# Performance work log

Measured on AMD Instinct MI355X. Metric: run time of the kernel, lower is better.

## Reference

```python
import jax, jax.numpy as jnp
import numpy as np

B, N, C = 8, 3072, 768
NUM_HEADS, NUM_DIL, KS = 12, 3, 3


def setup_inputs() -> dict:
    key = jax.random.key(0)
    k1, k2, k3 = jax.random.split(key, 3)
    x = jax.random.normal(k1, (B, N, C), dtype=jnp.float32)
    qkv_w = jax.random.normal(k2, (3 * C, C), dtype=jnp.float32) * 0.02
    proj_w = jax.random.normal(k3, (C, C), dtype=jnp.float32) * 0.02
    proj_b = jnp.zeros((C,), dtype=jnp.float32)
    return {"x": x, "qkv_w": qkv_w, "proj_w": proj_w, "proj_b": proj_b}


def reference(x, qkv_w, proj_w, proj_b):
    Bx, Nx, Cx = x.shape
    nd, ks, heads = NUM_DIL, KS, NUM_HEADS
    hd = Cx // heads          # head_dim = 64
    d = Cx // nd              # channels per dilation = 256
    h = heads // nd           # heads per dilation = 4
    nb = Nx // ks             # number of windows along N
    scale = hd ** -0.5

    # qkv: [B,N,3C] -> [nd,3,B,d,N] (matches torch permute(3,2,0,4,1))
    qkv = (x @ qkv_w.T).reshape(Bx, Nx, 3, nd, d)
    qkv = jnp.transpose(qkv, (3, 2, 0, 4, 1))
    q, k, v = qkv[:, 0], qkv[:, 1], qkv[:, 2]  # each [nd,B,d,N]

    def split_heads(t):
        # [nd,B,d,N] -> [nd,B,h,hd,ks,nb] -> [nd,B,h,nb,ks,hd]
        t = t.reshape(nd, Bx, h, hd, ks, nb)
        return jnp.transpose(t, (0, 1, 2, 5, 4, 3))

    qh = split_heads(q)
    kh = split_heads(k)
    vh = split_heads(v)

    # tiny per-window attention: [nd,B,h,nb,ks,ks]
    attn = jnp.einsum('nbhwqd,nbhwkd->nbhwqk', qh, kh) * scale
    attn = jax.nn.softmax(attn, axis=-1)
    out = jnp.einsum('nbhwqk,nbhwkd->nbhwqd', attn, vh)  # [nd,B,h,nb,ks,hd]

    # torch: transpose(1,2).reshape(B,N,d) per dilation, then permute(1,2,0,3).reshape(B,N,C)
    out = jnp.transpose(out, (0, 1, 3, 2, 4, 5)).reshape(nd, Bx, Nx, d)
    out = jnp.transpose(out, (1, 2, 0, 3)).reshape(Bx, Nx, Cx)
    return out @ proj_w.T + proj_b
```

## Files before the change

### kernel.cpp

```cpp
#include <hip/hip_runtime.h>
#include <stdint.h>

#define DEVFN __device__ __forceinline__

typedef unsigned short u16;
typedef __bf16 bf16_t;
typedef bf16_t bf16x8 __attribute__((ext_vector_type(8)));
typedef float  f32x4  __attribute__((ext_vector_type(4)));

static constexpr int Bb = 8, Nn = 3072, Cc = 768;
static constexpr int Mr = Bb * Nn;
static constexpr int C3 = 3 * Cc;
static constexpr int NB = 1024;

DEVFN u16 f2bf_rne(float f) {
  uint32_t u = __builtin_bit_cast(uint32_t, f);
  u += 0x7FFFu + ((u >> 16) & 1u);
  return (u16)(u >> 16);
}
DEVFN float bf2f(u16 v) {
  uint32_t u = ((uint32_t)v) << 16;
  return __builtin_bit_cast(float, u);
}

__global__ void cvt_f32_bf16(const float4* __restrict__ in, ushort4* __restrict__ out, int n4) {
  int i = blockIdx.x * blockDim.x + threadIdx.x;
  int stride = gridDim.x * blockDim.x;
  for (; i < n4; i += stride) {
    float4 v = in[i];
    ushort4 o;
    o.x = f2bf_rne(v.x); o.y = f2bf_rne(v.y);
    o.z = f2bf_rne(v.z); o.w = f2bf_rne(v.w);
    out[i] = o;
  }
}

DEVFN void gload_lds16(const void* g, void* l) {
  __builtin_amdgcn_global_load_lds(
      (const __attribute__((address_space(1))) uint32_t*)g,
      (__attribute__((address_space(3))) uint32_t*)l,
      16, 0, 0);
}

template <bool OUT_F32>
__global__ __launch_bounds__(512, 2)
void gemm256(const u16* __restrict__ A, const u16* __restrict__ Bw,
             void* __restrict__ Cout, const float* __restrict__ bias,
             int Ndim, int K) {
  constexpr int SLOT = 32768;
  __shared__ char lds[4 * SLOT];

  const int nTn = Ndim >> 8;
  const int nwg = gridDim.x;
  const int bid = blockIdx.x;
  const int wgid = (bid & 7) * (nwg >> 3) + (bid >> 3);
  const int tm = wgid / nTn, tn = wgid % nTn;

  const int t = threadIdx.x;
  const int l = t & 63;
  const int w = t >> 6;
  const int wr = w >> 2;
  const int wcq = w & 3;
  const int lr = l & 15;

  const int NPH = K >> 5;

  const int srow = l >> 2;
  const int scol = 8 * ((l & 3) ^ (srow & 3));
  const u16* pA0 = A  + (size_t)(tm * 256 +       w * 16 + srow) * K + scol;
  const u16* pA1 = A  + (size_t)(tm * 256 + 128 + w * 16 + srow) * K + scol;
  const u16* pB0 = Bw + (size_t)(tn * 256 +       w * 16 + srow) * K + scol;
  const u16* pB1 = Bw + (size_t)(tn * 256 + 128 + w * 16 + srow) * K + scol;

  const int lane_off = lr * 64 + (((l >> 4) * 16) ^ ((lr & 3) << 4));

  f32x4 acc[8][4];
  #pragma unroll
  for (int m = 0; m < 8; ++m)
    #pragma unroll
    for (int n = 0; n < 4; ++n)
      acc[m][n] = f32x4{0.f, 0.f, 0.f, 0.f};

  #pragma unroll
  for (int q = 0; q < 3; ++q) {
    char* dA = &lds[q * SLOT + w * 1024];
    char* dB = &lds[q * SLOT + 16384 + w * 1024];
    const size_t ko = (size_t)q * 32;
    gload_lds16(pA0 + ko, dA);
    gload_lds16(pA1 + ko, dA + 8192);
    gload_lds16(pB0 + ko, dB);
    gload_lds16(pB1 + ko, dB + 8192);
  }

#define GPHASE(VMSTR, PF_COND)                                                \
  do {                                                                        \
    asm volatile(VMSTR ::: "memory");                                         \
    __builtin_amdgcn_s_barrier();                                             \
    asm volatile("" ::: "memory");                                            \
    const char* ab = &lds[(p & 3) * SLOT] + wr * 8192 + lane_off;             \
    const char* bb = &lds[(p & 3) * SLOT + 16384] + wcq * 4096 + lane_off;    \
    bf16x8 af[8], bf[4];                                                      \
    _Pragma("unroll")                                                         \
    for (int m = 0; m < 8; ++m)                                               \
      af[m] = *reinterpret_cast<const bf16x8*>(ab + m * 1024);                \
    _Pragma("unroll")                                                         \
    for (int n = 0; n < 4; ++n)                                               \
      bf[n] = *reinterpret_cast<const bf16x8*>(bb + n * 1024);                \
    if (PF_COND) {                                                            \
      const int ps = (p + 3) & 3;                                             \
      char* dA = &lds[ps * SLOT + w * 1024];                                  \
      char* dB = &lds[ps * SLOT + 16384 + w * 1024];                          \
      const size_t ko = (size_t)(p + 3) * 32;                                 \
      gload_lds16(pA0 + ko, dA);                                              \
      gload_lds16(pA1 + ko, dA + 8192);                                       \
      gload_lds16(pB0 + ko, dB);                                              \
      gload_lds16(pB1 + ko, dB + 8192);                                       \
    }                                                                         \
    __builtin_amdgcn_s_setprio(1);                                            \
    _Pragma("unroll")                                                         \
    for (int m = 0; m < 8; ++m)                                               \
      _Pragma("unroll")                                                       \
      for (int n = 0; n < 4; ++n)                                             \
        acc[m][n] = __builtin_amdgcn_mfma_f32_16x16x32_bf16(af[m], bf[n],     \
                                                            acc[m][n], 0,0,0);\
    __builtin_amdgcn_s_setprio(0);                                            \
    asm volatile("" ::: "memory");                                            \
  } while (0)

  int p = 0;
  for (; p < NPH - 2; ++p) GPHASE("s_waitcnt vmcnt(8)", (p + 3 < NPH));
  GPHASE("s_waitcnt vmcnt(4)", false); ++p;
  GPHASE("s_waitcnt vmcnt(0)", false); ++p;
#undef GPHASE

  const int rb = tm * 256 + wr * 128 + (l >> 4) * 4;
  const int cbase = tn * 256 + wcq * 64 + lr;
  #pragma unroll
  for (int m = 0; m < 8; ++m) {
    #pragma unroll
    for (int n = 0; n < 4; ++n) {
      const int col = cbase + n * 16;
      const int row0 = rb + m * 16;
      if constexpr (OUT_F32) {
        float* O = (float*)Cout;
        const float bv = bias[col];
        #pragma unroll
        for (int j = 0; j < 4; ++j)
          O[(size_t)(row0 + j) * Ndim + col] = acc[m][n][j] + bv;
      } else {
        u16* O = (u16*)Cout;
        #pragma unroll
        for (int j = 0; j < 4; ++j)
          O[(size_t)(row0 + j) * Ndim + col] = f2bf_rne(acc[m][n][j]);
      }
    }
  }
}

__global__ __launch_bounds__(256)
void attn_local(const u16* __restrict__ qkv, u16* __restrict__ y) {
  const int t = threadIdx.x;
  const int wv = t >> 6, lane = t & 63;
  int wid = blockIdx.x * 4 + wv;
  const int w = wid & (NB - 1); wid >>= 10;
  const int head = wid & 3; wid >>= 2;
  const int b = wid & 7; wid >>= 3;
  const int dil = wid;

  const int colq = dil * 256 + head * 64 + lane;
  float q[3], k[3], v[3];
  #pragma unroll
  for (int i = 0; i < 3; ++i) {
    const size_t row = (size_t)(b * Nn + i * NB + w) * C3;
    q[i] = bf2f(qkv[row + colq]);
    k[i] = bf2f(qkv[row + 768 + colq]);
    v[i] = bf2f(qkv[row + 1536 + colq]);
  }

  float s[3][3];
  #pragma unroll
  for (int i = 0; i < 3; ++i)
    #pragma unroll
    for (int j = 0; j < 3; ++j) {
      float p = q[i] * k[j];
      #pragma unroll
      for (int off = 32; off > 0; off >>= 1)
        p += __shfl_xor(p, off, 64);
      s[i][j] = p * 0.125f;
    }

  #pragma unroll
  for (int i = 0; i < 3; ++i) {
    const float mx = fmaxf(fmaxf(s[i][0], s[i][1]), s[i][2]);
    const float e0 = __expf(s[i][0] - mx);
    const float e1 = __expf(s[i][1] - mx);
    const float e2 = __expf(s[i][2] - mx);
    const float inv = 1.0f / (e0 + e1 + e2);
    const float o = (e0 * v[0] + e1 * v[1] + e2 * v[2]) * inv;
    const int linear = head * 192 + i * 64 + lane;
    const int nout = w * 3 + (linear >> 8);
    const int dd = linear & 255;
    y[(size_t)(b * Nn + nout) * Cc + dil * 256 + dd] = f2bf_rne(o);
  }
}

extern "C" void kernel_launch(void* const* d_in, const int* in_sizes, int n_in,
                              void* d_out, int out_size, void* d_ws, size_t ws_size,
                              hipStream_t stream) {
  const float* x      = (const float*)d_in[0];
  const float* qkv_w  = (const float*)d_in[1];
  const float* proj_w = (const float*)d_in[2];
  const float* proj_b = (const float*)d_in[3];

  char* ws = (char*)d_ws;
  u16* wq_b = (u16*)(ws);
  u16* wp_b = (u16*)(ws + 3538944);
  u16* xb   = (u16*)(ws + 4718592);
  u16* qkvb = (u16*)(ws + 42467328);
  u16* yb   = xb;

  cvt_f32_bf16<<<2048, 256, 0, stream>>>((const float4*)x,      (ushort4*)xb,   Mr * Cc / 4);
  cvt_f32_bf16<<<512,  256, 0, stream>>>((const float4*)qkv_w,  (ushort4*)wq_b, C3 * Cc / 4);
  cvt_f32_bf16<<<256,  256, 0, stream>>>((const float4*)proj_w, (ushort4*)wp_b, Cc * Cc / 4);

  gemm256<false><<<(Mr / 256) * (C3 / 256), 512, 0, stream>>>(xb, wq_b, qkvb, nullptr, C3, Cc);

  attn_local<<<(3 * 8 * 4 * 1024) / 4, 256, 0, stream>>>(qkvb, yb);

  gemm256<true><<<(Mr / 256) * (Cc / 256), 512, 0, stream>>>(yb, wp_b, d_out, proj_b, Cc, Cc);
}
```

Baseline: 245.3 us.

## Swap MFMA operands for vectorized GEMM epilogue stores and adjust LDS swizzle

Swapping the A and B operands of the MFMA transposes each accumulator fragment, so every lane holds four consecutive columns of one row. The epilogue can then write float4 (fp32) or ushort4 (bf16) vectors instead of four scalar strided stores, and load the bias as a float4. The LDS XOR swizzle now keys on row bits 1-2 instead of 0-1, changing the bank-conflict pattern for the shared-memory reads. This is meant to cut global store transactions, at the risk of new LDS bank conflicts if the swizzle fits the read pattern worse.

Result: slower. 263.5 us (+7.4%).

```diff
diff --git a/kernel.cpp b/kernel.cpp
--- a/kernel.cpp
+++ b/kernel.cpp
@@ -66,13 +66,13 @@
   const int NPH = K >> 5;
 
   const int srow = l >> 2;
-  const int scol = 8 * ((l & 3) ^ (srow & 3));
+  const int scol = 8 * ((l & 3) ^ ((srow >> 1) & 3));
   const u16* pA0 = A  + (size_t)(tm * 256 +       w * 16 + srow) * K + scol;
   const u16* pA1 = A  + (size_t)(tm * 256 + 128 + w * 16 + srow) * K + scol;
   const u16* pB0 = Bw + (size_t)(tn * 256 +       w * 16 + srow) * K + scol;
   const u16* pB1 = Bw + (size_t)(tn * 256 + 128 + w * 16 + srow) * K + scol;
 
-  const int lane_off = lr * 64 + (((l >> 4) * 16) ^ ((lr & 3) << 4));
+  const int lane_off = lr * 64 + (((l >> 4) * 16) ^ (((lr >> 1) & 3) << 4));
 
   f32x4 acc[8][4];
   #pragma unroll
@@ -121,7 +121,7 @@
     for (int m = 0; m < 8; ++m)                                               \
       _Pragma("unroll")                                                       \
       for (int n = 0; n < 4; ++n)                                             \
-        acc[m][n] = __builtin_amdgcn_mfma_f32_16x16x32_bf16(af[m], bf[n],     \
+        acc[m][n] = __builtin_amdgcn_mfma_f32_16x16x32_bf16(bf[n], af[m],     \
                                                             acc[m][n], 0,0,0);\
     __builtin_amdgcn_s_setprio(0);                                            \
     asm volatile("" ::: "memory");                                            \
@@ -133,25 +133,31 @@
   GPHASE("s_waitcnt vmcnt(0)", false); ++p;
 #undef GPHASE
 
-  const int rb = tm * 256 + wr * 128 + (l >> 4) * 4;
-  const int cbase = tn * 256 + wcq * 64 + lr;
+  const int grow0 = tm * 256 + wr * 128 + lr;
+  const int gcol0 = tn * 256 + wcq * 64 + (l >> 4) * 4;
   #pragma unroll
   for (int m = 0; m < 8; ++m) {
+    const int row = grow0 + m * 16;
     #pragma unroll
     for (int n = 0; n < 4; ++n) {
-      const int col = cbase + n * 16;
-      const int row0 = rb + m * 16;
+      const int col = gcol0 + n * 16;
       if constexpr (OUT_F32) {
         float* O = (float*)Cout;
-        const float bv = bias[col];
-        #pragma unroll
-        for (int j = 0; j < 4; ++j)
-          O[(size_t)(row0 + j) * Ndim + col] = acc[m][n][j] + bv;
+        const float4 bv = *reinterpret_cast<const float4*>(&bias[col]);
+        float4 o;
+        o.x = acc[m][n][0] + bv.x;
+        o.y = acc[m][n][1] + bv.y;
+        o.z = acc[m][n][2] + bv.z;
+        o.w = acc[m][n][3] + bv.w;
+        *reinterpret_cast<float4*>(&O[(size_t)row * Ndim + col]) = o;
       } else {
         u16* O = (u16*)Cout;
-        #pragma unroll
-        for (int j = 0; j < 4; ++j)
-          O[(size_t)(row0 + j) * Ndim + col] = f2bf_rne(acc[m][n][j]);
+        ushort4 o;
+        o.x = f2bf_rne(acc[m][n][0]);
+        o.y = f2bf_rne(acc[m][n][1]);
+        o.z = f2bf_rne(acc[m][n][2]);
+        o.w = f2bf_rne(acc[m][n][3]);
+        *reinterpret_cast<ushort4*>(&O[(size_t)row * Ndim + col]) = o;
       }
     }
   }
```
